# Optimization experiments

Measured on AMD Instinct MI355X. Metric: run time of the kernel, lower is better.

## Reference

```python
import jax, jax.numpy as jnp
import numpy as np

B, L, T = 256, 256, 50  # batch, max_len, num_tags


def setup_inputs() -> dict:
    key = jax.random.key(0)
    k1, k2, k3 = jax.random.split(key, 3)
    feats = jax.random.normal(k1, (B, L, T), dtype=jnp.float32)
    trans_m = jax.random.normal(k2, (T, T), dtype=jnp.float32)
    tags = jax.random.randint(k3, (B, L), 0, T)
    mask = jnp.ones((B, L), dtype=jnp.int32)
    return {"feats": feats, "trans_m": trans_m, "tags": tags, "mask": mask}


def _normalizer(logits, trans_m, m):
    # logits: (L, B, T), m: (L, B) float mask
    alpha0 = logits[0]  # (B, T)

    def step(alpha, inp):
        emit, mt = inp  # (B, T), (B,)
        # (B, T_from, T_to) broadcast add, logsumexp over T_from
        tmp = alpha[:, :, None] + trans_m[None, :, :] + emit[:, None, :]
        new = jax.nn.logsumexp(tmp, axis=1)
        alpha = jnp.where(mt[:, None] > 0, new, alpha)
        return alpha, None

    alpha, _ = jax.lax.scan(step, alpha0, (logits[1:], m[1:]))
    return jax.nn.logsumexp(alpha, axis=1)  # (B,)


def _gold_score(logits, trans_m, tags_t, m):
    # logits: (L, B, T); tags_t: (L, B); m: (L, B)
    trans_sc = trans_m[tags_t[:-1], tags_t[1:]] * m[1:]  # (L-1, B)
    emit_sc = jnp.take_along_axis(logits, tags_t[:, :, None], axis=2)[..., 0] * m  # (L, B)
    return jnp.sum(trans_sc + emit_sc[:-1], axis=0) + emit_sc[-1]  # (B,)


def reference(feats, trans_m, tags, mask):
    # feats: (B, L, T) -> (L, B, T); include_start_end_trans=False
    logits = jnp.transpose(feats, (1, 0, 2))
    tags_t = tags.T
    m = mask.T.astype(feats.dtype)
    all_path = _normalizer(logits, trans_m, m)
    gold = _gold_score(logits, trans_m, tags_t, m)
    return all_path - gold  # (B,) loss per example
```

## Files before the change

### kernel.cpp

```cpp
#include <hip/hip_runtime.h>
#include <math.h>


#define TAGS 50
#define LEN 256
#define NB 256
#define HALF 128
#define INV_LN2 1.4426950408889634f
#define LN2 0.6931471805599453f

typedef __attribute__((ext_vector_type(8))) short bf16x8;
typedef __attribute__((ext_vector_type(4))) float f32x4;

#if __has_builtin(__builtin_amdgcn_exp2f)
#define EXP2F(x) __builtin_amdgcn_exp2f(x)
#else
#define EXP2F(x) exp2f(x)
#endif
#if __has_builtin(__builtin_amdgcn_logf)
#define LOG2F(x) __builtin_amdgcn_logf(x)
#else
#define LOG2F(x) log2f(x)
#endif
#if __has_builtin(__builtin_amdgcn_rcpf)
#define RCPF(x) __builtin_amdgcn_rcpf(x)
#else
#define RCPF(x) (1.0f / (x))
#endif

__device__ __forceinline__ float readlane_f(float v, int srclane) {
  return __builtin_bit_cast(float,
      __builtin_amdgcn_readlane(__builtin_bit_cast(int, v), srclane));
}

__device__ __forceinline__ int bf16pair(float lo, float hi) {
  unsigned lb = (__builtin_bit_cast(unsigned, lo) + 0x8000u) >> 16;
  unsigned hb = (__builtin_bit_cast(unsigned, hi) + 0x8000u) & 0xFFFF0000u;
  return (int)(hb | lb);
}

union U8 { int i[4]; bf16x8 v; };

#define WS_U(b)  ((b) * 64)
#define WS_W(b)  ((NB + (b)) * 64)
#define WS_SF(b) (2 * NB * 64 + (b))
#define WS_SB(b) (2 * NB * 64 + NB + (b))

__global__ __launch_bounds__(64) void crf_scan_kernel(
    const float* __restrict__ feats,
    const float* __restrict__ trans,
    const int*   __restrict__ mask,
    float*       __restrict__ ws)
{
  const int bid    = blockIdx.x;
  const bool is_fwd = bid < NB;
  const int b      = is_fwd ? bid : bid - NB;
  const int lane   = threadIdx.x;
  const int q      = lane >> 4;
  const int n      = lane & 15;

  __shared__ __align__(16) float fraw[HALF * TAGS];
  __shared__ __align__(16) float flexp[HALF * 64];
  __shared__ int ml[HALF];

  const int base_l = is_fwd ? 0 : HALF;
  const float* fb = feats + ((size_t)b * LEN + base_l) * TAGS;
  const int*   mb = mask + b * LEN + base_l;

  {
    const float4* fv = (const float4*)fb;
    for (int i = lane; i < (HALF * TAGS) / 4; i += 64) {
      float4 v4 = fv[i];
      v4.x *= INV_LN2; v4.y *= INV_LN2; v4.z *= INV_LN2; v4.w *= INV_LN2;
      *(float4*)&fraw[i * 4] = v4;
    }
    for (int i = lane; i < HALF; i += 64) ml[i] = mb[i];
  }
  __syncthreads();

  for (int l = 0; l < HALF; ++l) {
    float v = 0.0f;
    if (lane < TAGS) v = EXP2F(fraw[l * TAGS + lane]);
    flexp[l * 64 + lane] = v;
  }
  __syncthreads();

  U8 Afr[4][2];
#pragma unroll
  for (int t = 0; t < 4; ++t)
#pragma unroll
    for (int c = 0; c < 2; ++c)
#pragma unroll
      for (int r = 0; r < 4; ++r) {
        const int col = 16 * t + n;
        const int tag0 = 16 * c + 4 * q + r;
        const int tag1 = tag0 + 32;
        float e0 = 0.0f, e1 = 0.0f;
        if (col < TAGS) {
          if (tag0 < TAGS)
            e0 = EXP2F((is_fwd ? trans[tag0 * TAGS + col]
                               : trans[col * TAGS + tag0]) * INV_LN2);
          if (tag1 < TAGS)
            e1 = EXP2F((is_fwd ? trans[tag1 * TAGS + col]
                               : trans[col * TAGS + tag1]) * INV_LN2);
        }
        Afr[t][c].i[r] = bf16pair(e0, e1);
      }

  const f32x4 zero4 = {0.0f, 0.0f, 0.0f, 0.0f};

#define LDEH(l_, I_) (*(const f32x4*)&flexp[(l_) * 64 + 16 * (I_) + 4 * q])

  float va[16];
  float S;

  if (is_fwd) {
    const float r0 = RCPF(flexp[0]);
    {
      f32x4 i0 = LDEH(0, 0), i1 = LDEH(0, 1), i2 = LDEH(0, 2), i3 = LDEH(0, 3);
#pragma unroll
      for (int r = 0; r < 4; ++r) {
        va[r]      = i0[r] * r0;
        va[4 + r]  = i1[r] * r0;
        va[8 + r]  = i2[r] * r0;
        va[12 + r] = i3[r] * r0;
      }
    }
    S = fraw[0];

    f32x4 eh0 = LDEH(1, 0), eh1 = LDEH(1, 1), eh2 = LDEH(1, 2), eh3 = LDEH(1, 3);
    int m_nxt = ml[1];

#pragma unroll 2
    for (int l = 1; l < HALF; ++l) {
      const int m_cur = m_nxt;
      const int ln = (l + 1 < HALF) ? (l + 1) : (HALF - 1);

      const float cc = readlane_f(va[0], 0);
      const float rr = RCPF(cc);

      U8 B0, B1;
#pragma unroll
      for (int r = 0; r < 4; ++r) {
        B0.i[r] = bf16pair(va[r],     va[8 + r]);
        B1.i[r] = bf16pair(va[4 + r], va[12 + r]);
      }

      f32x4 d0 = __builtin_amdgcn_mfma_f32_16x16x32_bf16(Afr[0][1].v, B1.v, zero4, 0, 0, 0);
      f32x4 d1 = __builtin_amdgcn_mfma_f32_16x16x32_bf16(Afr[1][1].v, B1.v, zero4, 0, 0, 0);
      f32x4 d2 = __builtin_amdgcn_mfma_f32_16x16x32_bf16(Afr[2][1].v, B1.v, zero4, 0, 0, 0);
      f32x4 d3 = __builtin_amdgcn_mfma_f32_16x16x32_bf16(Afr[3][1].v, B1.v, zero4, 0, 0, 0);
      d0 = __builtin_amdgcn_mfma_f32_16x16x32_bf16(Afr[0][0].v, B0.v, d0, 0, 0, 0);
      d1 = __builtin_amdgcn_mfma_f32_16x16x32_bf16(Afr[1][0].v, B0.v, d1, 0, 0, 0);
      d2 = __builtin_amdgcn_mfma_f32_16x16x32_bf16(Afr[2][0].v, B0.v, d2, 0, 0, 0);
      d3 = __builtin_amdgcn_mfma_f32_16x16x32_bf16(Afr[3][0].v, B0.v, d3, 0, 0, 0);

      f32x4 en0 = LDEH(ln, 0), en1 = LDEH(ln, 1), en2 = LDEH(ln, 2), en3 = LDEH(ln, 3);
      const int m_n2 = ml[ln];

#pragma unroll
      for (int r = 0; r < 4; ++r) {
        va[r]      = ((m_cur > 0) ? d0[r] * eh0[r] : va[r])      * rr;
        va[4 + r]  = ((m_cur > 0) ? d1[r] * eh1[r] : va[4 + r])  * rr;
        va[8 + r]  = ((m_cur > 0) ? d2[r] * eh2[r] : va[8 + r])  * rr;
        va[12 + r] = ((m_cur > 0) ? d3[r] * eh3[r] : va[12 + r]) * rr;
      }
      S += LOG2F(cc);
      eh0 = en0; eh1 = en1; eh2 = en2; eh3 = en3;
      m_nxt = m_n2;
    }

    if (n == 0) {
#pragma unroll
      for (int I = 0; I < 4; ++I)
#pragma unroll
        for (int r = 0; r < 4; ++r)
          ws[WS_U(b) + 16 * I + 4 * q + r] = va[4 * I + r];
    }
    if (lane == 0) ws[WS_SF(b)] = S;
  } else {
#pragma unroll
    for (int I = 0; I < 4; ++I)
#pragma unroll
      for (int r = 0; r < 4; ++r)
        va[4 * I + r] = (16 * I + 4 * q + r < TAGS) ? 1.0f : 0.0f;
    S = 0.0f;

    f32x4 eh0 = LDEH(HALF - 1, 0), eh1 = LDEH(HALF - 1, 1),
          eh2 = LDEH(HALF - 1, 2), eh3 = LDEH(HALF - 1, 3);
    int m_nxt = ml[HALF - 1];

#pragma unroll 2
    for (int l = HALF - 1; l >= 0; --l) {
      const int m_cur = m_nxt;
      const int ln = (l > 0) ? (l - 1) : 0;

      const float cc = readlane_f(va[0], 0);
      const float rr = RCPF(cc);

      float x[16];
#pragma unroll
      for (int r = 0; r < 4; ++r) {
        x[r]      = va[r]      * eh0[r];
        x[4 + r]  = va[4 + r]  * eh1[r];
        x[8 + r]  = va[8 + r]  * eh2[r];
        x[12 + r] = va[12 + r] * eh3[r];
      }

      U8 B0, B1;
#pragma unroll
      for (int r = 0; r < 4; ++r) {
        B0.i[r] = bf16pair(x[r],     x[8 + r]);
        B1.i[r] = bf16pair(x[4 + r], x[12 + r]);
      }

      f32x4 d0 = __builtin_amdgcn_mfma_f32_16x16x32_bf16(Afr[0][1].v, B1.v, zero4, 0, 0, 0);
      f32x4 d1 = __builtin_amdgcn_mfma_f32_16x16x32_bf16(Afr[1][1].v, B1.v, zero4, 0, 0, 0);
      f32x4 d2 = __builtin_amdgcn_mfma_f32_16x16x32_bf16(Afr[2][1].v, B1.v, zero4, 0, 0, 0);
      f32x4 d3 = __builtin_amdgcn_mfma_f32_16x16x32_bf16(Afr[3][1].v, B1.v, zero4, 0, 0, 0);
      d0 = __builtin_amdgcn_mfma_f32_16x16x32_bf16(Afr[0][0].v, B0.v, d0, 0, 0, 0);
      d1 = __builtin_amdgcn_mfma_f32_16x16x32_bf16(Afr[1][0].v, B0.v, d1, 0, 0, 0);
      d2 = __builtin_amdgcn_mfma_f32_16x16x32_bf16(Afr[2][0].v, B0.v, d2, 0, 0, 0);
      d3 = __builtin_amdgcn_mfma_f32_16x16x32_bf16(Afr[3][0].v, B0.v, d3, 0, 0, 0);

      f32x4 en0 = LDEH(ln, 0), en1 = LDEH(ln, 1), en2 = LDEH(ln, 2), en3 = LDEH(ln, 3);
      const int m_n2 = ml[ln];

#pragma unroll
      for (int r = 0; r < 4; ++r) {
        va[r]      = ((m_cur > 0) ? d0[r] : va[r])      * rr;
        va[4 + r]  = ((m_cur > 0) ? d1[r] : va[4 + r])  * rr;
        va[8 + r]  = ((m_cur > 0) ? d2[r] : va[8 + r])  * rr;
        va[12 + r] = ((m_cur > 0) ? d3[r] : va[12 + r]) * rr;
      }
      S += LOG2F(cc);
      eh0 = en0; eh1 = en1; eh2 = en2; eh3 = en3;
      m_nxt = m_n2;
    }

    if (n == 0) {
#pragma unroll
      for (int I = 0; I < 4; ++I)
#pragma unroll
        for (int r = 0; r < 4; ++r)
          ws[WS_W(b) + 16 * I + 4 * q + r] = va[4 * I + r];
    }
    if (lane == 0) ws[WS_SB(b)] = S;
  }
#undef LDEH
}

__global__ __launch_bounds__(64) void crf_combine_kernel(
    const float* __restrict__ feats,
    const float* __restrict__ trans,
    const int*   __restrict__ tags,
    const int*   __restrict__ mask,
    const float* __restrict__ ws,
    float*       __restrict__ out)
{
  const int b = blockIdx.x;
  const int lane = threadIdx.x;

  float s = ws[WS_U(b) + lane] * ws[WS_W(b) + lane];
#pragma unroll
  for (int off = 32; off; off >>= 1) s += __shfl_xor(s, off, 64);

  const float* fb = feats + (size_t)b * (LEN * TAGS);
  const int*   tb = tags + b * LEN;
  const int*   mb = mask + b * LEN;
  float gp = 0.0f;
#pragma unroll
  for (int k = 0; k < 4; ++k) {
    const int p = lane + 64 * k;
    const int tg = tb[p];
    if (mb[p] > 0) {
      float vv = fb[p * TAGS + tg];
      if (p >= 1) vv += trans[tb[p - 1] * TAGS + tg];
      gp += vv;
    }
  }
#pragma unroll
  for (int off = 32; off; off >>= 1) gp += __shfl_xor(gp, off, 64);

  if (lane == 0) {
    const float Sf = ws[WS_SF(b)];
    const float Sb = ws[WS_SB(b)];
    out[b] = LN2 * (Sf + Sb + LOG2F(s)) - gp;
  }
}

extern "C" void kernel_launch(void* const* d_in, const int* in_sizes, int n_in,
                              void* d_out, int out_size, void* d_ws, size_t ws_size,
                              hipStream_t stream) {
  const float* feats = (const float*)d_in[0];
  const float* trans = (const float*)d_in[1];
  const int*   tags  = (const int*)d_in[2];
  const int*   mask  = (const int*)d_in[3];
  float* out = (float*)d_out;
  float* ws  = (float*)d_ws;

  crf_scan_kernel<<<2 * NB, 64, 0, stream>>>(feats, trans, mask, ws);
  crf_combine_kernel<<<NB, 64, 0, stream>>>(feats, trans, tags, mask, ws, out);
}
```

Before: 116.8 us.

## Fuse forward/backward scans and combine into one block per sequence

Replaces the two-kernel design (512 blocks running separate forward and backward half-scans, then a combine kernel) with one kernel of 256 blocks. Each block interleaves the forward and backward recurrences in a single loop, giving two independent MFMA chains to hide latency, and computes the gold score in-block from shared memory. It also exponentiates feats during the load into a padded LDS layout, dropping the separate exp pass and the second launch. In exchange each block does double the serial work with half the blocks, LDS use roughly doubles, and the gold emission term is now recovered through log2 of the exponentiated value, which may lose some precision.

```diff
diff --git a/kernel.cpp b/kernel.cpp
--- a/kernel.cpp
+++ b/kernel.cpp
@@ -5,7 +5,7 @@
 #define TAGS 50
 #define LEN 256
 #define NB 256
-#define HALF 128
+#define RSTRIDE 52
 #define INV_LN2 1.4426950408889634f
 #define LN2 0.6931471805599453f
 
@@ -41,51 +41,48 @@
 
 union U8 { int i[4]; bf16x8 v; };
 
-#define WS_U(b)  ((b) * 64)
-#define WS_W(b)  ((NB + (b)) * 64)
-#define WS_SF(b) (2 * NB * 64 + (b))
-#define WS_SB(b) (2 * NB * 64 + NB + (b))
-
-__global__ __launch_bounds__(64) void crf_scan_kernel(
+__global__ __launch_bounds__(64, 1) void crf_fused_kernel(
     const float* __restrict__ feats,
     const float* __restrict__ trans,
+    const int*   __restrict__ tags,
     const int*   __restrict__ mask,
-    float*       __restrict__ ws)
+    float*       __restrict__ out)
 {
-  const int bid    = blockIdx.x;
-  const bool is_fwd = bid < NB;
-  const int b      = is_fwd ? bid : bid - NB;
-  const int lane   = threadIdx.x;
-  const int q      = lane >> 4;
-  const int n      = lane & 15;
-
-  __shared__ __align__(16) float fraw[HALF * TAGS];
-  __shared__ __align__(16) float flexp[HALF * 64];
-  __shared__ int ml[HALF];
-
-  const int base_l = is_fwd ? 0 : HALF;
-  const float* fb = feats + ((size_t)b * LEN + base_l) * TAGS;
-  const int*   mb = mask + b * LEN + base_l;
+  const int b    = blockIdx.x;
+  const int lane = threadIdx.x;
+  const int q    = lane >> 4;
+  const int n    = lane & 15;
+
+  __shared__ __align__(16) float flexp[LEN * RSTRIDE + 16];
+  __shared__ int ml[LEN];
+  __shared__ int tl[LEN];
 
   {
-    const float4* fv = (const float4*)fb;
-    for (int i = lane; i < (HALF * TAGS) / 4; i += 64) {
-      float4 v4 = fv[i];
-      v4.x *= INV_LN2; v4.y *= INV_LN2; v4.z *= INV_LN2; v4.w *= INV_LN2;
-      *(float4*)&fraw[i * 4] = v4;
-    }
-    for (int i = lane; i < HALF; i += 64) ml[i] = mb[i];
+    const float4* fv = (const float4*)(feats + (size_t)b * LEN * TAGS);
+    for (int i4 = lane; i4 < (LEN * TAGS) / 4; i4 += 64) {
+      float4 v4 = fv[i4];
+      float vv[4] = {v4.x, v4.y, v4.z, v4.w};
+      const int base = i4 * 4;
+#pragma unroll
+      for (int e = 0; e < 4; ++e) {
+        const int idx = base + e;
+        const unsigned row =
+            (unsigned)(((unsigned long long)(unsigned)idx * 1374389535ull) >> 36);
+        const int col = idx - (int)row * 50;
+        flexp[row * RSTRIDE + col] = EXP2F(vv[e] * INV_LN2);
+      }
+    }
+    for (int i = lane; i < LEN; i += 64) {
+      flexp[i * RSTRIDE + 50] = 0.0f;
+      flexp[i * RSTRIDE + 51] = 0.0f;
+      ml[i] = mask[b * LEN + i];
+      tl[i] = tags[b * LEN + i];
+    }
+    if (lane < 16) flexp[LEN * RSTRIDE + lane] = 0.0f;
   }
   __syncthreads();
 
-  for (int l = 0; l < HALF; ++l) {
-    float v = 0.0f;
-    if (lane < TAGS) v = EXP2F(fraw[l * TAGS + lane]);
-    flexp[l * 64 + lane] = v;
-  }
-  __syncthreads();
-
-  U8 Afr[4][2];
+  U8 Af[4][2], Ab[4][2];
 #pragma unroll
   for (int t = 0; t < 4; ++t)
 #pragma unroll
@@ -95,198 +92,175 @@
         const int col = 16 * t + n;
         const int tag0 = 16 * c + 4 * q + r;
         const int tag1 = tag0 + 32;
-        float e0 = 0.0f, e1 = 0.0f;
+        float f0 = 0.0f, f1 = 0.0f, g0 = 0.0f, g1 = 0.0f;
         if (col < TAGS) {
-          if (tag0 < TAGS)
-            e0 = EXP2F((is_fwd ? trans[tag0 * TAGS + col]
-                               : trans[col * TAGS + tag0]) * INV_LN2);
-          if (tag1 < TAGS)
-            e1 = EXP2F((is_fwd ? trans[tag1 * TAGS + col]
-                               : trans[col * TAGS + tag1]) * INV_LN2);
+          if (tag0 < TAGS) {
+            f0 = EXP2F(trans[tag0 * TAGS + col] * INV_LN2);
+            g0 = EXP2F(trans[col * TAGS + tag0] * INV_LN2);
+          }
+          if (tag1 < TAGS) {
+            f1 = EXP2F(trans[tag1 * TAGS + col] * INV_LN2);
+            g1 = EXP2F(trans[col * TAGS + tag1] * INV_LN2);
+          }
         }
-        Afr[t][c].i[r] = bf16pair(e0, e1);
+        Af[t][c].i[r] = bf16pair(f0, f1);
+        Ab[t][c].i[r] = bf16pair(g0, g1);
       }
 
   const f32x4 zero4 = {0.0f, 0.0f, 0.0f, 0.0f};
 
-#define LDEH(l_, I_) (*(const f32x4*)&flexp[(l_) * 64 + 16 * (I_) + 4 * q])
-
-  float va[16];
-  float S;
-
-  if (is_fwd) {
+#define LDEH(l_, I_) (*(const f32x4*)&flexp[(l_) * RSTRIDE + 16 * (I_) + 4 * q])
+
+  float vaf[16], vab[16], Sf, Sb;
+
+  {
     const float r0 = RCPF(flexp[0]);
-    {
-      f32x4 i0 = LDEH(0, 0), i1 = LDEH(0, 1), i2 = LDEH(0, 2), i3 = LDEH(0, 3);
-#pragma unroll
-      for (int r = 0; r < 4; ++r) {
-        va[r]      = i0[r] * r0;
-        va[4 + r]  = i1[r] * r0;
-        va[8 + r]  = i2[r] * r0;
-        va[12 + r] = i3[r] * r0;
-      }
-    }
-    S = fraw[0];
-
-    f32x4 eh0 = LDEH(1, 0), eh1 = LDEH(1, 1), eh2 = LDEH(1, 2), eh3 = LDEH(1, 3);
-    int m_nxt = ml[1];
-
-#pragma unroll 2
-    for (int l = 1; l < HALF; ++l) {
-      const int m_cur = m_nxt;
-      const int ln = (l + 1 < HALF) ? (l + 1) : (HALF - 1);
-
-      const float cc = readlane_f(va[0], 0);
-      const float rr = RCPF(cc);
-
-      U8 B0, B1;
-#pragma unroll
-      for (int r = 0; r < 4; ++r) {
-        B0.i[r] = bf16pair(va[r],     va[8 + r]);
-        B1.i[r] = bf16pair(va[4 + r], va[12 + r]);
-      }
-
-      f32x4 d0 = __builtin_amdgcn_mfma_f32_16x16x32_bf16(Afr[0][1].v, B1.v, zero4, 0, 0, 0);
-      f32x4 d1 = __builtin_amdgcn_mfma_f32_16x16x32_bf16(Afr[1][1].v, B1.v, zero4, 0, 0, 0);
-      f32x4 d2 = __builtin_amdgcn_mfma_f32_16x16x32_bf16(Afr[2][1].v, B1.v, zero4, 0, 0, 0);
-      f32x4 d3 = __builtin_amdgcn_mfma_f32_16x16x32_bf16(Afr[3][1].v, B1.v, zero4, 0, 0, 0);
-      d0 = __builtin_amdgcn_mfma_f32_16x16x32_bf16(Afr[0][0].v, B0.v, d0, 0, 0, 0);
-      d1 = __builtin_amdgcn_mfma_f32_16x16x32_bf16(Afr[1][0].v, B0.v, d1, 0, 0, 0);
-      d2 = __builtin_amdgcn_mfma_f32_16x16x32_bf16(Afr[2][0].v, B0.v, d2, 0, 0, 0);
-      d3 = __builtin_amdgcn_mfma_f32_16x16x32_bf16(Afr[3][0].v, B0.v, d3, 0, 0, 0);
-
-      f32x4 en0 = LDEH(ln, 0), en1 = LDEH(ln, 1), en2 = LDEH(ln, 2), en3 = LDEH(ln, 3);
-      const int m_n2 = ml[ln];
-
-#pragma unroll
-      for (int r = 0; r < 4; ++r) {
-        va[r]      = ((m_cur > 0) ? d0[r] * eh0[r] : va[r])      * rr;
-        va[4 + r]  = ((m_cur > 0) ? d1[r] * eh1[r] : va[4 + r])  * rr;
-        va[8 + r]  = ((m_cur > 0) ? d2[r] * eh2[r] : va[8 + r])  * rr;
-        va[12 + r] = ((m_cur > 0) ? d3[r] * eh3[r] : va[12 + r]) * rr;
-      }
-      S += LOG2F(cc);
-      eh0 = en0; eh1 = en1; eh2 = en2; eh3 = en3;
-      m_nxt = m_n2;
-    }
-
-    if (n == 0) {
-#pragma unroll
-      for (int I = 0; I < 4; ++I)
-#pragma unroll
-        for (int r = 0; r < 4; ++r)
-          ws[WS_U(b) + 16 * I + 4 * q + r] = va[4 * I + r];
-    }
-    if (lane == 0) ws[WS_SF(b)] = S;
-  } else {
-#pragma unroll
-    for (int I = 0; I < 4; ++I)
-#pragma unroll
-      for (int r = 0; r < 4; ++r)
-        va[4 * I + r] = (16 * I + 4 * q + r < TAGS) ? 1.0f : 0.0f;
-    S = 0.0f;
-
-    f32x4 eh0 = LDEH(HALF - 1, 0), eh1 = LDEH(HALF - 1, 1),
-          eh2 = LDEH(HALF - 1, 2), eh3 = LDEH(HALF - 1, 3);
-    int m_nxt = ml[HALF - 1];
-
-#pragma unroll 2
-    for (int l = HALF - 1; l >= 0; --l) {
-      const int m_cur = m_nxt;
-      const int ln = (l > 0) ? (l - 1) : 0;
-
-      const float cc = readlane_f(va[0], 0);
-      const float rr = RCPF(cc);
-
-      float x[16];
-#pragma unroll
-      for (int r = 0; r < 4; ++r) {
-        x[r]      = va[r]      * eh0[r];
-        x[4 + r]  = va[4 + r]  * eh1[r];
-        x[8 + r]  = va[8 + r]  * eh2[r];
-        x[12 + r] = va[12 + r] * eh3[r];
-      }
-
-      U8 B0, B1;
-#pragma unroll
-      for (int r = 0; r < 4; ++r) {
-        B0.i[r] = bf16pair(x[r],     x[8 + r]);
-        B1.i[r] = bf16pair(x[4 + r], x[12 + r]);
-      }
-
-      f32x4 d0 = __builtin_amdgcn_mfma_f32_16x16x32_bf16(Afr[0][1].v, B1.v, zero4, 0, 0, 0);
-      f32x4 d1 = __builtin_amdgcn_mfma_f32_16x16x32_bf16(Afr[1][1].v, B1.v, zero4, 0, 0, 0);
-      f32x4 d2 = __builtin_amdgcn_mfma_f32_16x16x32_bf16(Afr[2][1].v, B1.v, zero4, 0, 0, 0);
-      f32x4 d3 = __builtin_amdgcn_mfma_f32_16x16x32_bf16(Afr[3][1].v, B1.v, zero4, 0, 0, 0);
-      d0 = __builtin_amdgcn_mfma_f32_16x16x32_bf16(Afr[0][0].v, B0.v, d0, 0, 0, 0);
-      d1 = __builtin_amdgcn_mfma_f32_16x16x32_bf16(Afr[1][0].v, B0.v, d1, 0, 0, 0);
-      d2 = __builtin_amdgcn_mfma_f32_16x16x32_bf16(Afr[2][0].v, B0.v, d2, 0, 0, 0);
-      d3 = __builtin_amdgcn_mfma_f32_16x16x32_bf16(Afr[3][0].v, B0.v, d3, 0, 0, 0);
-
-      f32x4 en0 = LDEH(ln, 0), en1 = LDEH(ln, 1), en2 = LDEH(ln, 2), en3 = LDEH(ln, 3);
-      const int m_n2 = ml[ln];
-
-#pragma unroll
-      for (int r = 0; r < 4; ++r) {
-        va[r]      = ((m_cur > 0) ? d0[r] : va[r])      * rr;
-        va[4 + r]  = ((m_cur > 0) ? d1[r] : va[4 + r])  * rr;
-        va[8 + r]  = ((m_cur > 0) ? d2[r] : va[8 + r])  * rr;
-        va[12 + r] = ((m_cur > 0) ? d3[r] : va[12 + r]) * rr;
-      }
-      S += LOG2F(cc);
-      eh0 = en0; eh1 = en1; eh2 = en2; eh3 = en3;
-      m_nxt = m_n2;
-    }
-
-    if (n == 0) {
-#pragma unroll
-      for (int I = 0; I < 4; ++I)
-#pragma unroll
-        for (int r = 0; r < 4; ++r)
-          ws[WS_W(b) + 16 * I + 4 * q + r] = va[4 * I + r];
-    }
-    if (lane == 0) ws[WS_SB(b)] = S;
-  }
+    f32x4 i0 = LDEH(0, 0), i1 = LDEH(0, 1), i2 = LDEH(0, 2), i3 = LDEH(0, 3);
+#pragma unroll
+    for (int r = 0; r < 4; ++r) {
+      vaf[r]      = i0[r] * r0;
+      vaf[4 + r]  = i1[r] * r0;
+      vaf[8 + r]  = i2[r] * r0;
+      vaf[12 + r] = (48 + 4 * q + r < TAGS) ? i3[r] * r0 : 0.0f;
+    }
+    Sf = LOG2F(flexp[0]);
+  }
+#pragma unroll
+  for (int r = 0; r < 4; ++r) {
+    vab[r] = 1.0f; vab[4 + r] = 1.0f; vab[8 + r] = 1.0f;
+    vab[12 + r] = (48 + 4 * q + r < TAGS) ? 1.0f : 0.0f;
+  }
+  Sb = 0.0f;
+
+  f32x4 ehf0 = LDEH(1, 0), ehf1 = LDEH(1, 1), ehf2 = LDEH(1, 2), ehf3 = LDEH(1, 3);
+  f32x4 ehb0 = LDEH(255, 0), ehb1 = LDEH(255, 1), ehb2 = LDEH(255, 2), ehb3 = LDEH(255, 3);
+  int mf = ml[1], mb = ml[255];
+
+  for (int k = 0; k < 127; ++k) {
+    const int lfn = (k + 2 < 128) ? (k + 2) : 127;
+    const int lbn = 254 - k;
+
+    const float ccf = readlane_f(vaf[0], 0);
+    const float rrf = RCPF(ccf);
+    U8 F0, F1;
+#pragma unroll
+    for (int r = 0; r < 4; ++r) {
+      F0.i[r] = bf16pair(vaf[r],     vaf[8 + r]);
+      F1.i[r] = bf16pair(vaf[4 + r], vaf[12 + r]);
+    }
+    f32x4 fa0 = __builtin_amdgcn_mfma_f32_16x16x32_bf16(Af[0][0].v, F0.v, zero4, 0, 0, 0);
+    f32x4 fa1 = __builtin_amdgcn_mfma_f32_16x16x32_bf16(Af[1][0].v, F0.v, zero4, 0, 0, 0);
+    f32x4 fa2 = __builtin_amdgcn_mfma_f32_16x16x32_bf16(Af[2][0].v, F0.v, zero4, 0, 0, 0);
+    f32x4 fa3 = __builtin_amdgcn_mfma_f32_16x16x32_bf16(Af[3][0].v, F0.v, zero4, 0, 0, 0);
+    f32x4 fb0 = __builtin_amdgcn_mfma_f32_16x16x32_bf16(Af[0][1].v, F1.v, zero4, 0, 0, 0);
+    f32x4 fb1 = __builtin_amdgcn_mfma_f32_16x16x32_bf16(Af[1][1].v, F1.v, zero4, 0, 0, 0);
+    f32x4 fb2 = __builtin_amdgcn_mfma_f32_16x16x32_bf16(Af[2][1].v, F1.v, zero4, 0, 0, 0);
+    f32x4 fb3 = __builtin_amdgcn_mfma_f32_16x16x32_bf16(Af[3][1].v, F1.v, zero4, 0, 0, 0);
+
+    const float ccb = readlane_f(vab[0], 0);
+    const float rrb = RCPF(ccb);
+    float x[16];
+#pragma unroll
+    for (int r = 0; r < 4; ++r) {
+      x[r]      = vab[r]      * ehb0[r];
+      x[4 + r]  = vab[4 + r]  * ehb1[r];
+      x[8 + r]  = vab[8 + r]  * ehb2[r];
+      x[12 + r] = vab[12 + r] * ehb3[r];
+    }
+    U8 G0, G1;
+#pragma unroll
+    for (int r = 0; r < 4; ++r) {
+      G0.i[r] = bf16pair(x[r],     x[8 + r]);
+      G1.i[r] = bf16pair(x[4 + r], x[12 + r]);
+    }
+    f32x4 ba0 = __builtin_amdgcn_mfma_f32_16x16x32_bf16(Ab[0][0].v, G0.v, zero4, 0, 0, 0);
+    f32x4 ba1 = __builtin_amdgcn_mfma_f32_16x16x32_bf16(Ab[1][0].v, G0.v, zero4, 0, 0, 0);
+    f32x4 ba2 = __builtin_amdgcn_mfma_f32_16x16x32_bf16(Ab[2][0].v, G0.v, zero4, 0, 0, 0);
+    f32x4 ba3 = __builtin_amdgcn_mfma_f32_16x16x32_bf16(Ab[3][0].v, G0.v, zero4, 0, 0, 0);
+    f32x4 bb0 = __builtin_amdgcn_mfma_f32_16x16x32_bf16(Ab[0][1].v, G1.v, zero4, 0, 0, 0);
+    f32x4 bb1 = __builtin_amdgcn_mfma_f32_16x16x32_bf16(Ab[1][1].v, G1.v, zero4, 0, 0, 0);
+    f32x4 bb2 = __builtin_amdgcn_mfma_f32_16x16x32_bf16(Ab[2][1].v, G1.v, zero4, 0, 0, 0);
+    f32x4 bb3 = __builtin_amdgcn_mfma_f32_16x16x32_bf16(Ab[3][1].v, G1.v, zero4, 0, 0, 0);
+
+    f32x4 nf0 = LDEH(lfn, 0), nf1 = LDEH(lfn, 1), nf2 = LDEH(lfn, 2), nf3 = LDEH(lfn, 3);
+    f32x4 nb0 = LDEH(lbn, 0), nb1 = LDEH(lbn, 1), nb2 = LDEH(lbn, 2), nb3 = LDEH(lbn, 3);
+    const int mfn = ml[lfn], mbn = ml[lbn];
+
+#pragma unroll
+    for (int r = 0; r < 4; ++r) {
+      vaf[r]      = ((mf > 0) ? (fa0[r] + fb0[r]) * ehf0[r] : vaf[r])      * rrf;
+      vaf[4 + r]  = ((mf > 0) ? (fa1[r] + fb1[r]) * ehf1[r] : vaf[4 + r])  * rrf;
+      vaf[8 + r]  = ((mf > 0) ? (fa2[r] + fb2[r]) * ehf2[r] : vaf[8 + r])  * rrf;
+      vaf[12 + r] = ((mf > 0) ? (fa3[r] + fb3[r]) * ehf3[r] : vaf[12 + r]) * rrf;
+      vab[r]      = ((mb > 0) ? (ba0[r] + bb0[r]) : vab[r])      * rrb;
+      vab[4 + r]  = ((mb > 0) ? (ba1[r] + bb1[r]) : vab[4 + r])  * rrb;
+      vab[8 + r]  = ((mb > 0) ? (ba2[r] + bb2[r]) : vab[8 + r])  * rrb;
+      vab[12 + r] = ((mb > 0) ? (ba3[r] + bb3[r]) : vab[12 + r]) * rrb;
+    }
+    Sf += LOG2F(ccf);
+    Sb += LOG2F(ccb);
+    ehf0 = nf0; ehf1 = nf1; ehf2 = nf2; ehf3 = nf3;
+    ehb0 = nb0; ehb1 = nb1; ehb2 = nb2; ehb3 = nb3;
+    mf = mfn; mb = mbn;
+  }
+
+  {
+    const float ccb = readlane_f(vab[0], 0);
+    const float rrb = RCPF(ccb);
+    float x[16];
+#pragma unroll
+    for (int r = 0; r < 4; ++r) {
+      x[r]      = vab[r]      * ehb0[r];
+      x[4 + r]  = vab[4 + r]  * ehb1[r];
+      x[8 + r]  = vab[8 + r]  * ehb2[r];
+      x[12 + r] = vab[12 + r] * ehb3[r];
+    }
+    U8 G0, G1;
+#pragma unroll
+    for (int r = 0; r < 4; ++r) {
+      G0.i[r] = bf16pair(x[r],     x[8 + r]);
+      G1.i[r] = bf16pair(x[4 + r], x[12 + r]);
+    }
+    f32x4 ba0 = __builtin_amdgcn_mfma_f32_16x16x32_bf16(Ab[0][0].v, G0.v, zero4, 0, 0, 0);
+    f32x4 ba1 = __builtin_amdgcn_mfma_f32_16x16x32_bf16(Ab[1][0].v, G0.v, zero4, 0, 0, 0);
+    f32x4 ba2 = __builtin_amdgcn_mfma_f32_16x16x32_bf16(Ab[2][0].v, G0.v, zero4, 0, 0, 0);
+    f32x4 ba3 = __builtin_amdgcn_mfma_f32_16x16x32_bf16(Ab[3][0].v, G0.v, zero4, 0, 0, 0);
+    f32x4 bb0 = __builtin_amdgcn_mfma_f32_16x16x32_bf16(Ab[0][1].v, G1.v, zero4, 0, 0, 0);
+    f32x4 bb1 = __builtin_amdgcn_mfma_f32_16x16x32_bf16(Ab[1][1].v, G1.v, zero4, 0, 0, 0);
+    f32x4 bb2 = __builtin_amdgcn_mfma_f32_16x16x32_bf16(Ab[2][1].v, G1.v, zero4, 0, 0, 0);
+    f32x4 bb3 = __builtin_amdgcn_mfma_f32_16x16x32_bf16(Ab[3][1].v, G1.v, zero4, 0, 0, 0);
+#pragma unroll
+    for (int r = 0; r < 4; ++r) {
+      vab[r]      = ((mb > 0) ? (ba0[r] + bb0[r]) : vab[r])      * rrb;
+      vab[4 + r]  = ((mb > 0) ? (ba1[r] + bb1[r]) : vab[4 + r])  * rrb;
+      vab[8 + r]  = ((mb > 0) ? (ba2[r] + bb2[r]) : vab[8 + r])  * rrb;
+      vab[12 + r] = ((mb > 0) ? (ba3[r] + bb3[r]) : vab[12 + r]) * rrb;
+    }
+    Sb += LOG2F(ccb);
+  }
+
+  float part = 0.0f;
+#pragma unroll
+  for (int i = 0; i < 16; ++i) part += vaf[i] * vab[i];
+  part += __shfl_xor(part, 16, 64);
+  part += __shfl_xor(part, 32, 64);
+
+  float gp = 0.0f;
+#pragma unroll
+  for (int kk = 0; kk < 4; ++kk) {
+    const int p = lane + 64 * kk;
+    const int tg = tl[p];
+    if (ml[p] > 0) {
+      float vv = LN2 * LOG2F(flexp[p * RSTRIDE + tg]);
+      if (p >= 1) vv += trans[tl[p - 1] * TAGS + tg];
+      gp += vv;
+    }
+  }
+#pragma unroll
+  for (int off = 32; off; off >>= 1) gp += __shfl_xor(gp, off, 64);
+
+  if (lane == 0) out[b] = LN2 * (Sf + Sb + LOG2F(part)) - gp;
 #undef LDEH
-}
-
-__global__ __launch_bounds__(64) void crf_combine_kernel(
-    const float* __restrict__ feats,
-    const float* __restrict__ trans,
-    const int*   __restrict__ tags,
-    const int*   __restrict__ mask,
-    const float* __restrict__ ws,
-    float*       __restrict__ out)
-{
-  const int b = blockIdx.x;
-  const int lane = threadIdx.x;
-
-  float s = ws[WS_U(b) + lane] * ws[WS_W(b) + lane];
-#pragma unroll
-  for (int off = 32; off; off >>= 1) s += __shfl_xor(s, off, 64);
-
-  const float* fb = feats + (size_t)b * (LEN * TAGS);
-  const int*   tb = tags + b * LEN;
-  const int*   mb = mask + b * LEN;
-  float gp = 0.0f;
-#pragma unroll
-  for (int k = 0; k < 4; ++k) {
-    const int p = lane + 64 * k;
-    const int tg = tb[p];
-    if (mb[p] > 0) {
-      float vv = fb[p * TAGS + tg];
-      if (p >= 1) vv += trans[tb[p - 1] * TAGS + tg];
-      gp += vv;
-    }
-  }
-#pragma unroll
-  for (int off = 32; off; off >>= 1) gp += __shfl_xor(gp, off, 64);
-
-  if (lane == 0) {
-    const float Sf = ws[WS_SF(b)];
-    const float Sb = ws[WS_SB(b)];
-    out[b] = LN2 * (Sf + Sb + LOG2F(s)) - gp;
-  }
 }
 
 extern "C" void kernel_launch(void* const* d_in, const int* in_sizes, int n_in,
@@ -297,8 +271,7 @@
   const int*   tags  = (const int*)d_in[2];
   const int*   mask  = (const int*)d_in[3];
   float* out = (float*)d_out;
-  float* ws  = (float*)d_ws;
-
-  crf_scan_kernel<<<2 * NB, 64, 0, stream>>>(feats, trans, mask, ws);
-  crf_combine_kernel<<<NB, 64, 0, stream>>>(feats, trans, tags, mask, ws, out);
-}
+  (void)d_ws; (void)ws_size;
+
+  crf_fused_kernel<<<NB, 64, 0, stream>>>(feats, trans, tags, mask, out);
+}
```

After: 154.4 us. 1.32x slower.

## Fuse exp into load, ballot masks, pack bf16 via cvt, renormalize every four steps

Applied to the files above, without the earlier changes.

Merges the feature load and exponentiation into one pass that writes a padded shared array with 52-float row stride. Masks are held in two wave ballots instead of shared memory, so each step branches on a uniform bit rather than selecting per element. bf16 packing now uses the hardware v_cvt_pk_bf16_f32 instruction, and the readlane/rcp/log2 renormalization runs once per four steps instead of every step, with double-buffered emission registers. This shortens the serial per-step dependency chain, but the longer gap between renormalizations risks overflow or underflow in the scaled values, and the ballot reads hardcode 128 steps per half.

```diff
diff --git a/kernel.cpp b/kernel.cpp
--- a/kernel.cpp
+++ b/kernel.cpp
@@ -6,6 +6,7 @@
 #define LEN 256
 #define NB 256
 #define HALF 128
+#define RS 52
 #define INV_LN2 1.4426950408889634f
 #define LN2 0.6931471805599453f
 
@@ -33,11 +34,14 @@
       __builtin_amdgcn_readlane(__builtin_bit_cast(int, v), srclane));
 }
 
-__device__ __forceinline__ int bf16pair(float lo, float hi) {
+__device__ __forceinline__ int bf16pairInit(float lo, float hi) {
   unsigned lb = (__builtin_bit_cast(unsigned, lo) + 0x8000u) >> 16;
   unsigned hb = (__builtin_bit_cast(unsigned, hi) + 0x8000u) & 0xFFFF0000u;
   return (int)(hb | lb);
 }
+
+#define PACK2(dst, lo, hi) \
+  asm("v_cvt_pk_bf16_f32 %0, %1, %2" : "=v"(dst) : "v"(lo), "v"(hi))
 
 union U8 { int i[4]; bf16x8 v; };
 
@@ -59,9 +63,7 @@
   const int q      = lane >> 4;
   const int n      = lane & 15;
 
-  __shared__ __align__(16) float fraw[HALF * TAGS];
-  __shared__ __align__(16) float flexp[HALF * 64];
-  __shared__ int ml[HALF];
+  __shared__ __align__(16) float flexp[HALF * RS + 16];
 
   const int base_l = is_fwd ? 0 : HALF;
   const float* fb = feats + ((size_t)b * LEN + base_l) * TAGS;
@@ -69,20 +71,27 @@
 
   {
     const float4* fv = (const float4*)fb;
-    for (int i = lane; i < (HALF * TAGS) / 4; i += 64) {
-      float4 v4 = fv[i];
-      v4.x *= INV_LN2; v4.y *= INV_LN2; v4.z *= INV_LN2; v4.w *= INV_LN2;
-      *(float4*)&fraw[i * 4] = v4;
-    }
-    for (int i = lane; i < HALF; i += 64) ml[i] = mb[i];
+    for (int i4 = lane; i4 < (HALF * TAGS) / 4; i4 += 64) {
+      float4 v4 = fv[i4];
+      float vv[4] = {v4.x, v4.y, v4.z, v4.w};
+      const int base = i4 * 4;
+#pragma unroll
+      for (int e = 0; e < 4; ++e) {
+        const int idx = base + e;
+        const unsigned row =
+            (unsigned)(((unsigned long long)(unsigned)idx * 1374389535ull) >> 36);
+        const int col = idx - (int)row * 50;
+        flexp[row * RS + col] = EXP2F(vv[e] * INV_LN2);
+      }
+    }
+    for (int i = lane; i < HALF; i += 64) {
+      flexp[i * RS + 50] = 0.0f;
+      flexp[i * RS + 51] = 0.0f;
+    }
+    if (lane < 16) flexp[HALF * RS + lane] = 0.0f;
   }
-  __syncthreads();
-
-  for (int l = 0; l < HALF; ++l) {
-    float v = 0.0f;
-    if (lane < TAGS) v = EXP2F(fraw[l * TAGS + lane]);
-    flexp[l * 64 + lane] = v;
-  }
+  const unsigned long long mball0 = __ballot(mb[lane] > 0);
+  const unsigned long long mball1 = __ballot(mb[64 + lane] > 0);
   __syncthreads();
 
   U8 Afr[4][2];
@@ -104,71 +113,118 @@
             e1 = EXP2F((is_fwd ? trans[tag1 * TAGS + col]
                                : trans[col * TAGS + tag1]) * INV_LN2);
         }
-        Afr[t][c].i[r] = bf16pair(e0, e1);
+        Afr[t][c].i[r] = bf16pairInit(e0, e1);
       }
 
   const f32x4 zero4 = {0.0f, 0.0f, 0.0f, 0.0f};
 
-#define LDEH(l_, I_) (*(const f32x4*)&flexp[(l_) * 64 + 16 * (I_) + 4 * q])
-
   float va[16];
-  float S;
+  float S = 0.0f;
+  f32x4 eA[4], eB[4];
+
+#define MASKBIT(L) \
+  ((int)(((((L) & 64) ? mball1 : mball0) >> ((L) & 63)) & 1ull))
+
+#define LOAD4(BK, ROW) do {                                   \
+    const float* _p = &flexp[(ROW) * RS + 4 * q];             \
+    BK[0] = *(const f32x4*)(_p);                              \
+    BK[1] = *(const f32x4*)(_p + 16);                         \
+    BK[2] = *(const f32x4*)(_p + 32);                         \
+    BK[3] = *(const f32x4*)(_p + 48);                         \
+  } while (0)
+
+#define RENORM() do {                                         \
+    const float _cc = readlane_f(va[0], 0);                   \
+    const float _rr = RCPF(_cc);                              \
+    S += LOG2F(_cc);                                          \
+    _Pragma("unroll") for (int _i = 0; _i < 16; ++_i) va[_i] *= _rr; \
+  } while (0)
+
+#define MFMA8(B0_, B1_)                                                        \
+    f32x4 d0 = __builtin_amdgcn_mfma_f32_16x16x32_bf16(Afr[0][1].v, B1_.v, zero4, 0, 0, 0); \
+    f32x4 d1 = __builtin_amdgcn_mfma_f32_16x16x32_bf16(Afr[1][1].v, B1_.v, zero4, 0, 0, 0); \
+    f32x4 d2 = __builtin_amdgcn_mfma_f32_16x16x32_bf16(Afr[2][1].v, B1_.v, zero4, 0, 0, 0); \
+    f32x4 d3 = __builtin_amdgcn_mfma_f32_16x16x32_bf16(Afr[3][1].v, B1_.v, zero4, 0, 0, 0); \
+    d0 = __builtin_amdgcn_mfma_f32_16x16x32_bf16(Afr[0][0].v, B0_.v, d0, 0, 0, 0);          \
+    d1 = __builtin_amdgcn_mfma_f32_16x16x32_bf16(Afr[1][0].v, B0_.v, d1, 0, 0, 0);          \
+    d2 = __builtin_amdgcn_mfma_f32_16x16x32_bf16(Afr[2][0].v, B0_.v, d2, 0, 0, 0);          \
+    d3 = __builtin_amdgcn_mfma_f32_16x16x32_bf16(Afr[3][0].v, B0_.v, d3, 0, 0, 0)
+
+#define FSTEP(EH, L, RL) do {                                 \
+    if (MASKBIT(L)) {                                         \
+      U8 B0, B1;                                              \
+      PACK2(B0.i[0], va[0], va[8]);                           \
+      PACK2(B0.i[1], va[1], va[9]);                           \
+      PACK2(B0.i[2], va[2], va[10]);                          \
+      PACK2(B0.i[3], va[3], va[11]);                          \
+      PACK2(B1.i[0], va[4], va[12]);                          \
+      PACK2(B1.i[1], va[5], va[13]);                          \
+      PACK2(B1.i[2], va[6], va[14]);                          \
+      PACK2(B1.i[3], va[7], va[15]);                          \
+      MFMA8(B0, B1);                                          \
+      _Pragma("unroll") for (int _r = 0; _r < 4; ++_r) {      \
+        va[_r]      = d0[_r] * EH[0][_r];                     \
+        va[4 + _r]  = d1[_r] * EH[1][_r];                     \
+        va[8 + _r]  = d2[_r] * EH[2][_r];                     \
+        va[12 + _r] = d3[_r] * EH[3][_r];                     \
+      }                                                       \
+    }                                                         \
+    LOAD4(EH, RL);                                            \
+  } while (0)
+
+#define BSTEP(EH, L, RL) do {                                 \
+    if (MASKBIT(L)) {                                         \
+      float x[16];                                            \
+      _Pragma("unroll") for (int _r = 0; _r < 4; ++_r) {      \
+        x[_r]      = va[_r]      * EH[0][_r];                 \
+        x[4 + _r]  = va[4 + _r]  * EH[1][_r];                 \
+        x[8 + _r]  = va[8 + _r]  * EH[2][_r];                 \
+        x[12 + _r] = va[12 + _r] * EH[3][_r];                 \
+      }                                                       \
+      U8 B0, B1;                                              \
+      PACK2(B0.i[0], x[0], x[8]);                             \
+      PACK2(B0.i[1], x[1], x[9]);                             \
+      PACK2(B0.i[2], x[2], x[10]);                            \
+      PACK2(B0.i[3], x[3], x[11]);                            \
+      PACK2(B1.i[0], x[4], x[12]);                            \
+      PACK2(B1.i[1], x[5], x[13]);                            \
+      PACK2(B1.i[2], x[6], x[14]);                            \
+      PACK2(B1.i[3], x[7], x[15]);                            \
+      MFMA8(B0, B1);                                          \
+      _Pragma("unroll") for (int _r = 0; _r < 4; ++_r) {      \
+        va[_r]      = d0[_r];                                 \
+        va[4 + _r]  = d1[_r];                                 \
+        va[8 + _r]  = d2[_r];                                 \
+        va[12 + _r] = d3[_r];                                 \
+      }                                                       \
+    }                                                         \
+    LOAD4(EH, RL);                                            \
+  } while (0)
 
   if (is_fwd) {
-    const float r0 = RCPF(flexp[0]);
-    {
-      f32x4 i0 = LDEH(0, 0), i1 = LDEH(0, 1), i2 = LDEH(0, 2), i3 = LDEH(0, 3);
-#pragma unroll
-      for (int r = 0; r < 4; ++r) {
-        va[r]      = i0[r] * r0;
-        va[4 + r]  = i1[r] * r0;
-        va[8 + r]  = i2[r] * r0;
-        va[12 + r] = i3[r] * r0;
-      }
-    }
-    S = fraw[0];
-
-    f32x4 eh0 = LDEH(1, 0), eh1 = LDEH(1, 1), eh2 = LDEH(1, 2), eh3 = LDEH(1, 3);
-    int m_nxt = ml[1];
-
-#pragma unroll 2
-    for (int l = 1; l < HALF; ++l) {
-      const int m_cur = m_nxt;
-      const int ln = (l + 1 < HALF) ? (l + 1) : (HALF - 1);
-
-      const float cc = readlane_f(va[0], 0);
-      const float rr = RCPF(cc);
-
-      U8 B0, B1;
-#pragma unroll
-      for (int r = 0; r < 4; ++r) {
-        B0.i[r] = bf16pair(va[r],     va[8 + r]);
-        B1.i[r] = bf16pair(va[4 + r], va[12 + r]);
-      }
-
-      f32x4 d0 = __builtin_amdgcn_mfma_f32_16x16x32_bf16(Afr[0][1].v, B1.v, zero4, 0, 0, 0);
-      f32x4 d1 = __builtin_amdgcn_mfma_f32_16x16x32_bf16(Afr[1][1].v, B1.v, zero4, 0, 0, 0);
-      f32x4 d2 = __builtin_amdgcn_mfma_f32_16x16x32_bf16(Afr[2][1].v, B1.v, zero4, 0, 0, 0);
-      f32x4 d3 = __builtin_amdgcn_mfma_f32_16x16x32_bf16(Afr[3][1].v, B1.v, zero4, 0, 0, 0);
-      d0 = __builtin_amdgcn_mfma_f32_16x16x32_bf16(Afr[0][0].v, B0.v, d0, 0, 0, 0);
-      d1 = __builtin_amdgcn_mfma_f32_16x16x32_bf16(Afr[1][0].v, B0.v, d1, 0, 0, 0);
-      d2 = __builtin_amdgcn_mfma_f32_16x16x32_bf16(Afr[2][0].v, B0.v, d2, 0, 0, 0);
-      d3 = __builtin_amdgcn_mfma_f32_16x16x32_bf16(Afr[3][0].v, B0.v, d3, 0, 0, 0);
-
-      f32x4 en0 = LDEH(ln, 0), en1 = LDEH(ln, 1), en2 = LDEH(ln, 2), en3 = LDEH(ln, 3);
-      const int m_n2 = ml[ln];
-
-#pragma unroll
-      for (int r = 0; r < 4; ++r) {
-        va[r]      = ((m_cur > 0) ? d0[r] * eh0[r] : va[r])      * rr;
-        va[4 + r]  = ((m_cur > 0) ? d1[r] * eh1[r] : va[4 + r])  * rr;
-        va[8 + r]  = ((m_cur > 0) ? d2[r] * eh2[r] : va[8 + r])  * rr;
-        va[12 + r] = ((m_cur > 0) ? d3[r] * eh3[r] : va[12 + r]) * rr;
-      }
-      S += LOG2F(cc);
-      eh0 = en0; eh1 = en1; eh2 = en2; eh3 = en3;
-      m_nxt = m_n2;
-    }
+    LOAD4(eA, 0);
+#pragma unroll
+    for (int r = 0; r < 4; ++r) {
+      va[r]      = eA[0][r];
+      va[4 + r]  = eA[1][r];
+      va[8 + r]  = eA[2][r];
+      va[12 + r] = (48 + 4 * q + r < TAGS) ? eA[3][r] : 0.0f;
+    }
+    LOAD4(eA, 1);
+    LOAD4(eB, 2);
+
+    for (int k = 0; k < 31; ++k) {
+      const int l0 = 4 * k + 1;
+      RENORM();
+      FSTEP(eA, l0,     l0 + 2);
+      FSTEP(eB, l0 + 1, l0 + 3);
+      FSTEP(eA, l0 + 2, l0 + 4);
+      FSTEP(eB, l0 + 3, l0 + 5);
+    }
+    RENORM();
+    FSTEP(eA, 125, 127);
+    FSTEP(eB, 126, 127);
+    FSTEP(eA, 127, 127);
 
     if (n == 0) {
 #pragma unroll
@@ -180,62 +236,20 @@
     if (lane == 0) ws[WS_SF(b)] = S;
   } else {
 #pragma unroll
-    for (int I = 0; I < 4; ++I)
-#pragma unroll
-      for (int r = 0; r < 4; ++r)
-        va[4 * I + r] = (16 * I + 4 * q + r < TAGS) ? 1.0f : 0.0f;
-    S = 0.0f;
-
-    f32x4 eh0 = LDEH(HALF - 1, 0), eh1 = LDEH(HALF - 1, 1),
-          eh2 = LDEH(HALF - 1, 2), eh3 = LDEH(HALF - 1, 3);
-    int m_nxt = ml[HALF - 1];
-
-#pragma unroll 2
-    for (int l = HALF - 1; l >= 0; --l) {
-      const int m_cur = m_nxt;
-      const int ln = (l > 0) ? (l - 1) : 0;
-
-      const float cc = readlane_f(va[0], 0);
-      const float rr = RCPF(cc);
-
-      float x[16];
-#pragma unroll
-      for (int r = 0; r < 4; ++r) {
-        x[r]      = va[r]      * eh0[r];
-        x[4 + r]  = va[4 + r]  * eh1[r];
-        x[8 + r]  = va[8 + r]  * eh2[r];
-        x[12 + r] = va[12 + r] * eh3[r];
-      }
-
-      U8 B0, B1;
-#pragma unroll
-      for (int r = 0; r < 4; ++r) {
-        B0.i[r] = bf16pair(x[r],     x[8 + r]);
-        B1.i[r] = bf16pair(x[4 + r], x[12 + r]);
-      }
-
-      f32x4 d0 = __builtin_amdgcn_mfma_f32_16x16x32_bf16(Afr[0][1].v, B1.v, zero4, 0, 0, 0);
-      f32x4 d1 = __builtin_amdgcn_mfma_f32_16x16x32_bf16(Afr[1][1].v, B1.v, zero4, 0, 0, 0);
-      f32x4 d2 = __builtin_amdgcn_mfma_f32_16x16x32_bf16(Afr[2][1].v, B1.v, zero4, 0, 0, 0);
-      f32x4 d3 = __builtin_amdgcn_mfma_f32_16x16x32_bf16(Afr[3][1].v, B1.v, zero4, 0, 0, 0);
-      d0 = __builtin_amdgcn_mfma_f32_16x16x32_bf16(Afr[0][0].v, B0.v, d0, 0, 0, 0);
-      d1 = __builtin_amdgcn_mfma_f32_16x16x32_bf16(Afr[1][0].v, B0.v, d1, 0, 0, 0);
-      d2 = __builtin_amdgcn_mfma_f32_16x16x32_bf16(Afr[2][0].v, B0.v, d2, 0, 0, 0);
-      d3 = __builtin_amdgcn_mfma_f32_16x16x32_bf16(Afr[3][0].v, B0.v, d3, 0, 0, 0);
-
-      f32x4 en0 = LDEH(ln, 0), en1 = LDEH(ln, 1), en2 = LDEH(ln, 2), en3 = LDEH(ln, 3);
-      const int m_n2 = ml[ln];
-
-#pragma unroll
-      for (int r = 0; r < 4; ++r) {
-        va[r]      = ((m_cur > 0) ? d0[r] : va[r])      * rr;
-        va[4 + r]  = ((m_cur > 0) ? d1[r] : va[4 + r])  * rr;
-        va[8 + r]  = ((m_cur > 0) ? d2[r] : va[8 + r])  * rr;
-        va[12 + r] = ((m_cur > 0) ? d3[r] : va[12 + r]) * rr;
-      }
-      S += LOG2F(cc);
-      eh0 = en0; eh1 = en1; eh2 = en2; eh3 = en3;
-      m_nxt = m_n2;
+    for (int r = 0; r < 4; ++r) {
+      va[r] = 1.0f; va[4 + r] = 1.0f; va[8 + r] = 1.0f;
+      va[12 + r] = (48 + 4 * q + r < TAGS) ? 1.0f : 0.0f;
+    }
+    LOAD4(eA, 127);
+    LOAD4(eB, 126);
+
+    for (int k = 0; k < 32; ++k) {
+      const int l0 = 127 - 4 * k;
+      RENORM();
+      BSTEP(eA, l0,     (l0 - 2 >= 0) ? l0 - 2 : 0);
+      BSTEP(eB, l0 - 1, (l0 - 3 >= 0) ? l0 - 3 : 0);
+      BSTEP(eA, l0 - 2, (l0 - 4 >= 0) ? l0 - 4 : 0);
+      BSTEP(eB, l0 - 3, (l0 - 5 >= 0) ? l0 - 5 : 0);
     }
 
     if (n == 0) {
@@ -247,7 +261,12 @@
     }
     if (lane == 0) ws[WS_SB(b)] = S;
   }
-#undef LDEH
+#undef MASKBIT
+#undef LOAD4
+#undef RENORM
+#undef MFMA8
+#undef FSTEP
+#undef BSTEP
 }
 
 __global__ __launch_bounds__(64) void crf_combine_kernel(
```

Result: faster. 106.4 us (-8.9%).
